# Optimization experiments

Hardware: AMD Instinct MI355X
Metric: run time of the kernel (lower is better)

The kernel has to match this reference:

```python
import jax, jax.numpy as jnp
import numpy as np

DN = ('NCHW', 'OIHW', 'NCHW')
B, H, W = 2048, 16, 16
DICT, SE, CE, ESZ, NZ = 14, 8, 16, 512, 512
EPS = 1e-4


def _conv(x, w, b):
    # 3x3 conv, padding=1 (SAME), NCHW
    return jax.lax.conv_general_dilated(x, w, (1, 1), 'SAME', dimension_numbers=DN) + b[None, :, None, None]


def _normalized(m, eps=0.0):
    return m / (jnp.sqrt(jnp.sum(m * m, axis=1, keepdims=True)) + eps)


def setup_inputs() -> dict:
    key = jax.random.key(0)
    ks = jax.random.split(key, 20)
    f = jnp.float32
    d = {
        's': jax.random.randint(ks[0], (B, H, W), 0, DICT, dtype=jnp.int32),
        's_prime': jax.random.randint(ks[1], (B, H, W), 0, DICT, dtype=jnp.int32),
        'state_embed': jax.random.normal(ks[2], (DICT, SE), f),
        'conv_embed_w': jax.random.normal(ks[3], (CE, SE, 3, 3), f) * 0.1,
        'conv_embed_b': jnp.zeros((CE,), f),
        'p1c1_w': jax.random.normal(ks[4], (16, CE, 3, 3), f) * 0.1,
        'p1c1_b': jnp.zeros((16,), f),
        'p1c2_w': jax.random.normal(ks[5], (32, 16, 3, 3), f) * 0.1,
        'p1c2_b': jnp.zeros((32,), f),
        'p1l_w': jax.random.normal(ks[6], (ESZ, 32 * H * W), f) * 0.02,
        'p1l_b': jnp.zeros((ESZ,), f),
        'p2c1_w': jax.random.normal(ks[7], (16, CE, 3, 3), f) * 0.1,
        'p2c1_b': jnp.zeros((16,), f),
        'p2c2_w': jax.random.normal(ks[8], (32, 16, 3, 3), f) * 0.1,
        'p2c2_b': jnp.zeros((32,), f),
        'p2l_w': jax.random.normal(ks[9], (ESZ, 32 * H * W), f) * 0.02,
        'p2l_b': jnp.zeros((ESZ,), f),
        'z_vectors': jax.random.normal(ks[10], (NZ, ESZ), f),
        'scale': jnp.ones((1,), f),
        'downscale_factor': 1,
    }
    return d


def _embed(s, state_embed, conv_embed_w, conv_embed_b):
    # nn.Embedding(max_norm=1): renorm rows to L2 norm <= 1 before lookup
    norms = jnp.sqrt(jnp.sum(state_embed * state_embed, axis=1, keepdims=True))
    table = state_embed / jnp.maximum(norms, 1.0)
    x = table[s]  # (B, H, W, SE)
    x = jnp.transpose(x, (0, 3, 1, 2))  # (B, SE, H, W)
    return _conv(x, conv_embed_w, conv_embed_b)


def _tower(x, c1w, c1b, c2w, c2b, lw, lb):
    x = jax.nn.relu(_conv(x, c1w, c1b))
    x = jax.nn.relu(_conv(x, c2w, c2b))
    x = x.reshape(x.shape[0], -1)  # (B, 32*H*W)
    x = x @ lw.T + lb
    return _normalized(x, EPS)


def reference(s, s_prime, state_embed, conv_embed_w, conv_embed_b,
              p1c1_w, p1c1_b, p1c2_w, p1c2_b, p1l_w, p1l_b,
              p2c1_w, p2c1_b, p2c2_w, p2c2_b, p2l_w, p2l_b,
              z_vectors, scale, downscale_factor):
    s_e = _embed(s, state_embed, conv_embed_w, conv_embed_b)
    sp_e = _embed(s_prime, state_embed, conv_embed_w, conv_embed_b)
    embed1 = _tower(s_e, p1c1_w, p1c1_b, p1c2_w, p1c2_b, p1l_w, p1l_b)
    embed2 = _tower(sp_e - s_e, p2c1_w, p2c1_b, p2c2_w, p2c2_b, p2l_w, p2l_b)
    # VQ: cosine-similarity nearest codebook vector
    zn = _normalized(z_vectors, 0.0)  # (NZ, ESZ)
    z_inds = jnp.argmax(embed2 @ zn.T, axis=1)  # (B,)
    z_matrix = zn[z_inds]  # (B, ESZ)
    if downscale_factor == 1:
        ipm = embed1 @ z_matrix.T  # (B, B)
    else:
        bs = embed1.shape[0] // downscale_factor
        v1 = embed1[::downscale_factor]  # (bs, ESZ)
        v2 = z_matrix.reshape(bs, downscale_factor, -1)
        ipm = jnp.einsum('be,bde->bd', v1, v2)
    return jnp.exp(scale) * ipm
```

## Files before the change

### kernel.cpp

```cpp
#include <hip/hip_runtime.h>
#include <math.h>


typedef __attribute__((ext_vector_type(8))) __bf16 bf16x8;
typedef __attribute__((ext_vector_type(4))) float f32x4;
typedef __attribute__((ext_vector_type(8))) unsigned short ushort8;
typedef __attribute__((ext_vector_type(4))) unsigned short ushort4v;

static __device__ __forceinline__ unsigned short f2bf(float x) {
  union { float f; unsigned u; } v; v.f = x;
  return (unsigned short)(v.u >> 16);
}
static __device__ __forceinline__ float bf2f(unsigned short h) {
  union { float f; unsigned u; } v; v.u = ((unsigned)h) << 16;
  return v.f;
}
template<int NS>
static __device__ __forceinline__ void split3(float x, unsigned short* h) {
  unsigned short q0 = f2bf(x); h[0] = q0;
  float r1 = x - bf2f(q0);
  unsigned short q1 = f2bf(r1); h[1] = q1;
  if constexpr (NS == 3) h[2] = f2bf(r1 - bf2f(q1));
}
static __device__ __forceinline__ void gload_lds16(const void* g, void* l) {
  __builtin_amdgcn_global_load_lds(
      (const __attribute__((address_space(1))) unsigned int*)g,
      (__attribute__((address_space(3))) unsigned int*)l, 16, 0, 0);
}
#define MFMA16(a, b, c) __builtin_amdgcn_mfma_f32_16x16x32_bf16((a), (b), (c), 0, 0, 0)

template<int NS>
static __device__ __forceinline__ f32x4 mfma_prod(const bf16x8* a, const bf16x8* b, f32x4 c) {
  c = MFMA16(a[0], b[0], c);
  c = MFMA16(a[0], b[1], c);
  c = MFMA16(a[1], b[0], c);
  if constexpr (NS == 3) {
    c = MFMA16(a[1], b[1], c);
    c = MFMA16(a[0], b[2], c);
    c = MFMA16(a[2], b[0], c);
  }
  return c;
}
static __device__ __forceinline__ int conv_a16(int cell, int half) {
  return (cell * 2 + half) ^ ((cell >> 2) & 7);
}
static __device__ __forceinline__ unsigned long long score_key(float v, int col) {
  unsigned b = __float_as_uint(v);
  unsigned m = b ^ ((unsigned)((int)b >> 31) | 0x80000000u);
  return ((unsigned long long)m << 32) | (unsigned)(511 - col);
}
static __device__ __forceinline__ unsigned long long shfl_xor_u64(unsigned long long v, int m) {
  unsigned lo = __shfl_xor((unsigned)v, m, 64);
  unsigned hi = __shfl_xor((unsigned)(v >> 32), m, 64);
  return ((unsigned long long)hi << 32) | lo;
}

__global__ __launch_bounds__(256) void prep_misc_kernel(
    const float* __restrict__ se, float* __restrict__ tbl,
    const float* __restrict__ zv,
    unsigned short* __restrict__ zn0, unsigned short* __restrict__ zn1,
    unsigned short* __restrict__ zn2,
    float* __restrict__ epre, unsigned long long* __restrict__ zi)
{
  __shared__ float wsum[4];
  const int b = blockIdx.x, t = threadIdx.x;
  if (b == 0) {
    if (t < 112) {
      int r = t >> 3;
      float ss = 0.f;
      #pragma unroll
      for (int i = 0; i < 8; ++i) { float v = se[r * 8 + i]; ss += v * v; }
      float n = fmaxf(sqrtf(ss), 1.0f);
      tbl[t] = se[t] / n;
    }
  } else if (b <= 512) {
    int row = b - 1;
    size_t base = (size_t)row * 512 + t * 2;
    float2 v = *reinterpret_cast<const float2*>(zv + base);
    float ss = v.x * v.x + v.y * v.y;
    #pragma unroll
    for (int m = 32; m >= 1; m >>= 1) ss += __shfl_xor(ss, m, 64);
    int lane = t & 63, wid = t >> 6;
    if (lane == 0) wsum[wid] = ss;
    __syncthreads();
    float tot = wsum[0] + wsum[1] + wsum[2] + wsum[3];
    float inv = 1.0f / sqrtf(tot);
    float a = v.x * inv, c = v.y * inv;
    unsigned short ha[3], hc[3];
    split3<3>(a, ha); split3<3>(c, hc);
    zn0[base] = ha[0]; zn0[base + 1] = hc[0];
    zn1[base] = ha[1]; zn1[base + 1] = hc[1];
    zn2[base] = ha[2]; zn2[base + 1] = hc[2];
  } else if (b <= 1024) {
    f32x4 z4 = {0.f, 0.f, 0.f, 0.f};
    size_t o = ((size_t)(b - 513) * 256 + t) * 8;
    *reinterpret_cast<f32x4*>(epre + o) = z4;
    *reinterpret_cast<f32x4*>(epre + o + 4) = z4;
  } else {
    int i = (b - 1025) * 256 + t;
    if (i < 2048) zi[i] = 0ull;
  }
}

__global__ __launch_bounds__(256) void prep_wt_all_kernel(
    const float* __restrict__ ew,
    const float* __restrict__ p1c1w, const float* __restrict__ p1c2w,
    const float* __restrict__ p2c1w, const float* __restrict__ p2c2w,
    unsigned short* __restrict__ wt)
{
  int gi = blockIdx.x * 256 + threadIdx.x;
  if (gi >= 50688) return;
  const float* src; int off, NSs, OC, mode;
  if (gi < 4608)       { src = ew;    off = 0;     NSs = 3; OC = 16; mode = 0; }
  else if (gi < 12288) { src = p1c1w; off = 4608;  NSs = 5; OC = 16; mode = 1; }
  else if (gi < 27648) { src = p1c2w; off = 12288; NSs = 5; OC = 32; mode = 1; }
  else if (gi < 35328) { src = p2c1w; off = 27648; NSs = 5; OC = 16; mode = 1; }
  else                 { src = p2c2w; off = 35328; NSs = 5; OC = 32; mode = 1; }
  int i = gi - off;
  int ic = i & 7;
  int r = i >> 3;
  int oc = r % OC; r /= OC;
  int kc = r & 3; r >>= 2;
  int s = r % NSs;
  int sp = r / NSs;
  int tap, icf, IC;
  if (mode == 0) { tap = s * 4 + kc; icf = ic; IC = 8; }
  else           { tap = s * 2 + (kc >> 1); icf = (kc & 1) * 8 + ic; IC = 16; }
  float w = 0.f;
  if (tap < 9) {
    int ky = tap / 3, kx = tap - ky * 3;
    w = src[((oc * IC + icf) * 3 + ky) * 3 + kx];
  }
  unsigned short h[3];
  split3<3>(w, h);
  wt[gi] = h[sp];
}

__global__ __launch_bounds__(256) void split_lin_kernel(
    const float* __restrict__ p1, const float* __restrict__ p2,
    unsigned short* __restrict__ w0, unsigned short* __restrict__ w1,
    unsigned short* __restrict__ u0, unsigned short* __restrict__ u1,
    unsigned short* __restrict__ u2)
{
  int blk = blockIdx.x;
  if (blk < 4096) {
    size_t i = ((size_t)blk * 256 + threadIdx.x) * 4;
    f32x4 v = *reinterpret_cast<const f32x4*>(p1 + i);
    ushort4v a, b;
    #pragma unroll
    for (int j = 0; j < 4; ++j) {
      unsigned short h[3];
      split3<2>(v[j], h);
      a[j] = h[0]; b[j] = h[1];
    }
    *reinterpret_cast<ushort4v*>(w0 + i) = a;
    *reinterpret_cast<ushort4v*>(w1 + i) = b;
  } else {
    size_t i = ((size_t)(blk - 4096) * 256 + threadIdx.x) * 4;
    f32x4 v = *reinterpret_cast<const f32x4*>(p2 + i);
    ushort4v a, b, c;
    #pragma unroll
    for (int j = 0; j < 4; ++j) {
      unsigned short h[3];
      split3<3>(v[j], h);
      a[j] = h[0]; b[j] = h[1]; c[j] = h[2];
    }
    *reinterpret_cast<ushort4v*>(u0 + i) = a;
    *reinterpret_cast<ushort4v*>(u1 + i) = b;
    *reinterpret_cast<ushort4v*>(u2 + i) = c;
  }
}

__global__ __launch_bounds__(256) void reduce_norm_kernel(
    const float* __restrict__ pre, const float* __restrict__ bias, float eps,
    unsigned short* __restrict__ o0, unsigned short* __restrict__ o1,
    unsigned short* __restrict__ o2, float* __restrict__ zero_dst)
{
  int row = blockIdx.x, t = threadIdx.x;
  size_t base = (size_t)row * 512 + t * 2;
  float2 v = *reinterpret_cast<const float2*>(pre + base);
  float ax = v.x + bias[t * 2], ay = v.y + bias[t * 2 + 1];
  float ss = ax * ax + ay * ay;
  #pragma unroll
  for (int m = 32; m >= 1; m >>= 1) ss += __shfl_xor(ss, m, 64);
  __shared__ float wsum[4];
  int lane = t & 63, wid = t >> 6;
  if (lane == 0) wsum[wid] = ss;
  __syncthreads();
  float tot = wsum[0] + wsum[1] + wsum[2] + wsum[3];
  float inv = 1.0f / (sqrtf(tot) + eps);
  float a = ax * inv, b2 = ay * inv;
  unsigned short ha[3], hb[3];
  split3<3>(a, ha); split3<3>(b2, hb);
  o0[base] = ha[0]; o0[base + 1] = hb[0];
  o1[base] = ha[1]; o1[base + 1] = hb[1];
  if (o2) { o2[base] = ha[2]; o2[base + 1] = hb[2]; }
  if (zero_dst) {
    float2 z = {0.f, 0.f};
    *reinterpret_cast<float2*>(zero_dst + base) = z;
  }
}

template<int NS>
__global__ __launch_bounds__(256) void tower_mfma_kernel(
    const int* __restrict__ sIdx, const int* __restrict__ spIdx,
    const float* __restrict__ tblf,
    const unsigned short* __restrict__ wtE,
    const unsigned short* __restrict__ wt1,
    const unsigned short* __restrict__ wt2,
    const float* __restrict__ eb, const float* __restrict__ c1b,
    const float* __restrict__ c2b,
    unsigned short* __restrict__ a0, unsigned short* __restrict__ a1,
    unsigned short* __restrict__ a2, int delta)
{
  __shared__ float tbl[112];
  __shared__ ushort8 G[NS][324];
  __shared__ ushort8 Abuf[NS][648];
  __shared__ ushort8 Bbuf[NS][648];

  const int b = blockIdx.x, t = threadIdx.x;
  const int lane = t & 63, wv = t >> 6;
  const int fr = lane & 15, kc = lane >> 4;

  if (t < 112) tbl[t] = tblf[t];
  if (t < 68) {
    int c;
    if (t < 18)      c = t;
    else if (t < 36) c = 306 + (t - 18);
    else if (t < 52) c = 18 * (t - 35);
    else             c = 18 * (t - 51) + 17;
    ushort8 z8 = {0, 0, 0, 0, 0, 0, 0, 0};
    #pragma unroll
    for (int sp = 0; sp < NS; ++sp) {
      G[sp][c] = z8;
      ((ushort8*)&Abuf[sp][0])[conv_a16(c, 0)] = z8;
      ((ushort8*)&Abuf[sp][0])[conv_a16(c, 1)] = z8;
      ((ushort8*)&Bbuf[sp][0])[conv_a16(c, 0)] = z8;
      ((ushort8*)&Bbuf[sp][0])[conv_a16(c, 1)] = z8;
    }
  }
  __syncthreads();

  {
    const int y = t >> 4, x = t & 15;
    const int cell = (y + 1) * 18 + (x + 1);
    int sv = sIdx[(size_t)b * 256 + t];
    float v[8];
    if (delta) {
      int spv = spIdx[(size_t)b * 256 + t];
      #pragma unroll
      for (int c = 0; c < 8; ++c) v[c] = tbl[spv * 8 + c] - tbl[sv * 8 + c];
    } else {
      #pragma unroll
      for (int c = 0; c < 8; ++c) v[c] = tbl[sv * 8 + c];
    }
    ushort8 h0, h1, h2;
    #pragma unroll
    for (int c = 0; c < 8; ++c) {
      unsigned short q[3];
      split3<NS>(v[c], q);
      h0[c] = q[0]; h1[c] = q[1];
      if constexpr (NS == 3) h2[c] = q[2];
    }
    G[0][cell] = h0; G[1][cell] = h1;
    if constexpr (NS == 3) G[2][cell] = h2;
  }
  __syncthreads();

  {
    float bias = 0.f;
    if (!delta) bias = eb[fr];
    f32x4 acc[4];
    #pragma unroll
    for (int j = 0; j < 4; ++j) acc[j] = (f32x4)0.f;
    #pragma unroll
    for (int s = 0; s < 3; ++s) {
      bf16x8 bw[NS];
      #pragma unroll
      for (int sp = 0; sp < NS; ++sp)
        bw[sp] = __builtin_bit_cast(bf16x8, *reinterpret_cast<const ushort8*>(
            wtE + (size_t)(((sp * 3 + s) * 4 + kc) * 16 + fr) * 8));
      int tap = s * 4 + kc; if (tap > 8) tap = 8;
      const int dy = tap / 3, dx = tap - dy * 3;
      const int cb = dy * 18 + fr + dx;
      #pragma unroll
      for (int j = 0; j < 4; ++j) {
        const int cell = cb + (wv * 4 + j) * 18;
        bf16x8 av[NS];
        #pragma unroll
        for (int sp = 0; sp < NS; ++sp)
          av[sp] = __builtin_bit_cast(bf16x8, G[sp][cell]);
        acc[j] = mfma_prod<NS>(av, bw, acc[j]);
      }
    }
    #pragma unroll
    for (int j = 0; j < 4; ++j) {
      const int y = wv * 4 + j;
      #pragma unroll
      for (int q = 0; q < 4; ++q) {
        const int x = kc * 4 + q;
        const int cell = (y + 1) * 18 + (x + 1);
        const int a16 = conv_a16(cell, fr >> 3);
        unsigned short hh[3];
        split3<NS>(acc[j][q] + bias, hh);
        #pragma unroll
        for (int sp = 0; sp < NS; ++sp)
          ((unsigned short*)&Abuf[sp][0])[a16 * 8 + (fr & 7)] = hh[sp];
      }
    }
  }
  __syncthreads();

  {
    const float bias = c1b[fr];
    f32x4 acc[4];
    #pragma unroll
    for (int j = 0; j < 4; ++j) acc[j] = (f32x4)0.f;
    #pragma unroll
    for (int s = 0; s < 5; ++s) {
      bf16x8 bw[NS];
      #pragma unroll
      for (int sp = 0; sp < NS; ++sp)
        bw[sp] = __builtin_bit_cast(bf16x8, *reinterpret_cast<const ushort8*>(
            wt1 + (size_t)(((sp * 5 + s) * 4 + kc) * 16 + fr) * 8));
      int tap = s * 2 + (kc >> 1); if (tap > 8) tap = 8;
      const int dy = tap / 3, dx = tap - dy * 3;
      const int half = kc & 1;
      const int cb = dy * 18 + fr + dx;
      #pragma unroll
      for (int j = 0; j < 4; ++j) {
        const int cell = cb + (wv * 4 + j) * 18;
        const int a16 = conv_a16(cell, half);
        bf16x8 av[NS];
        #pragma unroll
        for (int sp = 0; sp < NS; ++sp)
          av[sp] = __builtin_bit_cast(bf16x8, *reinterpret_cast<const ushort8*>(
              (const unsigned short*)&Abuf[sp][0] + a16 * 8));
        acc[j] = mfma_prod<NS>(av, bw, acc[j]);
      }
    }
    #pragma unroll
    for (int j = 0; j < 4; ++j) {
      const int y = wv * 4 + j;
      #pragma unroll
      for (int q = 0; q < 4; ++q) {
        const int x = kc * 4 + q;
        const int cell = (y + 1) * 18 + (x + 1);
        const int a16 = conv_a16(cell, fr >> 3);
        unsigned short hh[3];
        split3<NS>(fmaxf(acc[j][q] + bias, 0.f), hh);
        #pragma unroll
        for (int sp = 0; sp < NS; ++sp)
          ((unsigned short*)&Bbuf[sp][0])[a16 * 8 + (fr & 7)] = hh[sp];
      }
    }
  }
  __syncthreads();

  {
    const float bias0 = c2b[fr], bias1 = c2b[16 + fr];
    f32x4 acc0[4], acc1[4];
    #pragma unroll
    for (int j = 0; j < 4; ++j) { acc0[j] = (f32x4)0.f; acc1[j] = (f32x4)0.f; }
    #pragma unroll
    for (int s = 0; s < 5; ++s) {
      bf16x8 bw0[NS], bw1[NS];
      #pragma unroll
      for (int sp = 0; sp < NS; ++sp) {
        size_t base = (size_t)(((sp * 5 + s) * 4 + kc) * 32) * 8;
        bw0[sp] = __builtin_bit_cast(bf16x8,
            *reinterpret_cast<const ushort8*>(wt2 + base + (size_t)fr * 8));
        bw1[sp] = __builtin_bit_cast(bf16x8,
            *reinterpret_cast<const ushort8*>(wt2 + base + (size_t)(16 + fr) * 8));
      }
      int tap = s * 2 + (kc >> 1); if (tap > 8) tap = 8;
      const int dy = tap / 3, dx = tap - dy * 3;
      const int half = kc & 1;
      const int cb = dy * 18 + fr + dx;
      #pragma unroll
      for (int j = 0; j < 4; ++j) {
        const int cell = cb + (wv * 4 + j) * 18;
        const int a16 = conv_a16(cell, half);
        bf16x8 av[NS];
        #pragma unroll
        for (int sp = 0; sp < NS; ++sp)
          av[sp] = __builtin_bit_cast(bf16x8, *reinterpret_cast<const ushort8*>(
              (const unsigned short*)&Bbuf[sp][0] + a16 * 8));
        acc0[j] = mfma_prod<NS>(av, bw0, acc0[j]);
        acc1[j] = mfma_prod<NS>(av, bw1, acc1[j]);
      }
    }
    #pragma unroll
    for (int j = 0; j < 4; ++j) {
      const int y = wv * 4 + j;
      ushort4v g0[2], g1[2], g2[2];
      #pragma unroll
      for (int q = 0; q < 4; ++q) {
        unsigned short hh[3];
        split3<NS>(fmaxf(acc0[j][q] + bias0, 0.f), hh);
        g0[0][q] = hh[0]; g1[0][q] = hh[1]; if constexpr (NS == 3) g2[0][q] = hh[2];
        split3<NS>(fmaxf(acc1[j][q] + bias1, 0.f), hh);
        g0[1][q] = hh[0]; g1[1][q] = hh[1]; if constexpr (NS == 3) g2[1][q] = hh[2];
      }
      size_t base0 = (size_t)b * 8192 + (size_t)fr * 256 + y * 16 + kc * 4;
      size_t base1 = base0 + 16 * 256;
      *reinterpret_cast<ushort4v*>(a0 + base0) = g0[0];
      *reinterpret_cast<ushort4v*>(a0 + base1) = g0[1];
      *reinterpret_cast<ushort4v*>(a1 + base0) = g1[0];
      *reinterpret_cast<ushort4v*>(a1 + base1) = g1[1];
      if constexpr (NS == 3) {
        *reinterpret_cast<ushort4v*>(a2 + base0) = g2[0];
        *reinterpret_cast<ushort4v*>(a2 + base1) = g2[1];
      }
    }
  }
}

template<int NS, int EPI>
__global__ __launch_bounds__(256) void mfma_gemm_kernel(
    const unsigned short* __restrict__ A0, const unsigned short* __restrict__ A1,
    const unsigned short* __restrict__ A2,
    const unsigned short* __restrict__ B0, const unsigned short* __restrict__ B1,
    const unsigned short* __restrict__ B2,
    const unsigned long long* __restrict__ gkey,
    unsigned long long* __restrict__ zout,
    const float* __restrict__ scale_p,
    float* __restrict__ C, int M, int N, int K, int Ksub)
{
  __shared__ unsigned short ldsA[NS][4096];
  __shared__ unsigned short ldsB[NS][4096];

  const int t = threadIdx.x;
  const int lane = t & 63, wv = t >> 6;
  const int m0 = blockIdx.x * 128, n0 = blockIdx.y * 128;
  const long kbase = (long)blockIdx.z * Ksub;
  const int NT = Ksub >> 5;

  const int st_row = lane >> 2;
  const int st_cb = (lane & 3) * 16;
  int srow[2];
  long bgrow[2];
  #pragma unroll
  for (int r = 0; r < 2; ++r) {
    srow[r] = (wv + 4 * r) * 16 + st_row;
    long g = n0 + srow[r];
    if constexpr (EPI == 2)
      g = 511 - (long)(unsigned)(gkey[n0 + srow[r]] & 0xFFFFFFFFull);
    bgrow[r] = g;
  }

  const int wr = wv >> 1, wc = wv & 1;
  const int fr = lane & 15, kc = lane >> 4;

  f32x4 acc[4][4];
  #pragma unroll
  for (int mi = 0; mi < 4; ++mi)
    #pragma unroll
    for (int ni = 0; ni < 4; ++ni) acc[mi][ni] = (f32x4)0.f;

  const unsigned short* Asp[3] = {A0, A1, A2};
  const unsigned short* Bsp[3] = {B0, B1, B2};

  for (int kt = 0; kt < NT; ++kt) {
    const long k0 = kbase + (long)kt * 32;
    #pragma unroll
    for (int sp = 0; sp < NS; ++sp)
      #pragma unroll
      for (int r = 0; r < 2; ++r) {
        int row = srow[r];
        int c = st_cb ^ (((row >> 1) & 3) << 4);
        gload_lds16(Asp[sp] + (size_t)(m0 + row) * K + k0 + (c >> 1),
                    &ldsA[sp][(wv + 4 * r) * 512]);
      }
    #pragma unroll
    for (int sp = 0; sp < NS; ++sp)
      #pragma unroll
      for (int r = 0; r < 2; ++r) {
        int row = srow[r];
        int c = st_cb ^ (((row >> 1) & 3) << 4);
        gload_lds16(Bsp[sp] + (size_t)bgrow[r] * K + k0 + (c >> 1),
                    &ldsB[sp][(wv + 4 * r) * 512]);
      }
    __syncthreads();

    bf16x8 af[NS][4], bf[NS][4];
    #pragma unroll
    for (int sp = 0; sp < NS; ++sp) {
      #pragma unroll
      for (int mi = 0; mi < 4; ++mi) {
        int row = wr * 64 + mi * 16 + fr;
        int cb = (kc * 16) ^ (((row >> 1) & 3) << 4);
        af[sp][mi] = __builtin_bit_cast(bf16x8,
            *reinterpret_cast<const ushort8*>(&ldsA[sp][row * 32 + (cb >> 1)]));
      }
      #pragma unroll
      for (int ni = 0; ni < 4; ++ni) {
        int row = wc * 64 + ni * 16 + fr;
        int cb = (kc * 16) ^ (((row >> 1) & 3) << 4);
        bf[sp][ni] = __builtin_bit_cast(bf16x8,
            *reinterpret_cast<const ushort8*>(&ldsB[sp][row * 32 + (cb >> 1)]));
      }
    }
    #pragma unroll
    for (int mi = 0; mi < 4; ++mi)
      #pragma unroll
      for (int ni = 0; ni < 4; ++ni) {
        f32x4 c = acc[mi][ni];
        c = MFMA16(af[0][mi], bf[0][ni], c);
        c = MFMA16(af[0][mi], bf[1][ni], c);
        c = MFMA16(af[1][mi], bf[0][ni], c);
        if constexpr (NS == 3) {
          c = MFMA16(af[1][mi], bf[1][ni], c);
          c = MFMA16(af[0][mi], bf[2][ni], c);
          c = MFMA16(af[2][mi], bf[0][ni], c);
        }
        acc[mi][ni] = c;
      }
    __syncthreads();
  }

  if constexpr (EPI == 0) {
    #pragma unroll
    for (int mi = 0; mi < 4; ++mi)
      #pragma unroll
      for (int ni = 0; ni < 4; ++ni) {
        int col = n0 + wc * 64 + ni * 16 + fr;
        #pragma unroll
        for (int q = 0; q < 4; ++q) {
          int row = m0 + wr * 64 + mi * 16 + kc * 4 + q;
          atomicAdd(&C[(size_t)row * N + col], acc[mi][ni][q]);
        }
      }
  } else if constexpr (EPI == 2) {
    float scl = expf(scale_p[0]);
    #pragma unroll
    for (int mi = 0; mi < 4; ++mi)
      #pragma unroll
      for (int ni = 0; ni < 4; ++ni) {
        int col = n0 + wc * 64 + ni * 16 + fr;
        #pragma unroll
        for (int q = 0; q < 4; ++q) {
          int row = m0 + wr * 64 + mi * 16 + kc * 4 + q;
          C[(size_t)row * N + col] = acc[mi][ni][q] * scl;
        }
      }
  } else {
    #pragma unroll
    for (int mi = 0; mi < 4; ++mi)
      #pragma unroll
      for (int q = 0; q < 4; ++q) {
        int row = m0 + wr * 64 + mi * 16 + kc * 4 + q;
        unsigned long long best = 0ull;
        #pragma unroll
        for (int ni = 0; ni < 4; ++ni) {
          int col = n0 + wc * 64 + ni * 16 + fr;
          unsigned long long k2 = score_key(acc[mi][ni][q], col);
          best = (k2 > best) ? k2 : best;
        }
        #pragma unroll
        for (int m2 = 1; m2 < 16; m2 <<= 1) {
          unsigned long long o = shfl_xor_u64(best, m2);
          best = (o > best) ? o : best;
        }
        if (fr == 0) atomicMax(zout + row, best);
      }
  }
}

extern "C" void kernel_launch(void* const* d_in, const int* in_sizes, int n_in,
                              void* d_out, int out_size, void* d_ws, size_t ws_size,
                              hipStream_t stream)
{
  const int*   s      = (const int*)  d_in[0];
  const int*   sprime = (const int*)  d_in[1];
  const float* se     = (const float*)d_in[2];
  const float* ew     = (const float*)d_in[3];
  const float* eb     = (const float*)d_in[4];
  const float* p1c1w  = (const float*)d_in[5];
  const float* p1c1b  = (const float*)d_in[6];
  const float* p1c2w  = (const float*)d_in[7];
  const float* p1c2b  = (const float*)d_in[8];
  const float* p1lw   = (const float*)d_in[9];
  const float* p1lb   = (const float*)d_in[10];
  const float* p2c1w  = (const float*)d_in[11];
  const float* p2c1b  = (const float*)d_in[12];
  const float* p2c2w  = (const float*)d_in[13];
  const float* p2c2b  = (const float*)d_in[14];
  const float* p2lw   = (const float*)d_in[15];
  const float* p2lb   = (const float*)d_in[16];
  const float* zv     = (const float*)d_in[17];
  const float* scale  = (const float*)d_in[18];
  float* out = (float*)d_out;

  char* w = (char*)d_ws;
  size_t off = 0;
  auto alloc = [&](size_t bytes) -> char* {
    char* p = w + off;
    off += (bytes + 255) & ~(size_t)255;
    return p;
  };
  float* tblf = (float*)alloc(112 * 4);
  unsigned short* zn0 = (unsigned short*)alloc((size_t)512 * 512 * 2);
  unsigned short* zn1 = (unsigned short*)alloc((size_t)512 * 512 * 2);
  unsigned short* zn2 = (unsigned short*)alloc((size_t)512 * 512 * 2);
  unsigned short* e10 = (unsigned short*)alloc((size_t)2048 * 512 * 2);
  unsigned short* e11 = (unsigned short*)alloc((size_t)2048 * 512 * 2);
  unsigned short* e20 = (unsigned short*)alloc((size_t)2048 * 512 * 2);
  unsigned short* e21 = (unsigned short*)alloc((size_t)2048 * 512 * 2);
  unsigned short* e22 = (unsigned short*)alloc((size_t)2048 * 512 * 2);
  float* epre = (float*)alloc((size_t)2048 * 512 * 4);
  unsigned long long* zi = (unsigned long long*)alloc(2048 * 8);
  unsigned short* wt = (unsigned short*)alloc((size_t)50688 * 2);
  unsigned short* act0 = (unsigned short*)alloc((size_t)2048 * 8192 * 2);
  unsigned short* act1 = (unsigned short*)alloc((size_t)2048 * 8192 * 2);
  unsigned short* act2 = (unsigned short*)alloc((size_t)2048 * 8192 * 2);
  unsigned short* u0 = (unsigned short*)alloc((size_t)512 * 8192 * 2);
  unsigned short* u1 = (unsigned short*)alloc((size_t)512 * 8192 * 2);
  unsigned short* u2 = (unsigned short*)alloc((size_t)512 * 8192 * 2);
  unsigned short* w0 = act2;
  unsigned short* w1 = act2 + (size_t)512 * 8192;

  unsigned short* wtE  = wt;
  unsigned short* wt1a = wt + 4608;
  unsigned short* wt2a = wt + 12288;
  unsigned short* wt1b = wt + 27648;
  unsigned short* wt2b = wt + 35328;

  prep_misc_kernel<<<1033, 256, 0, stream>>>(se, tblf, zv, zn0, zn1, zn2, epre, zi);
  prep_wt_all_kernel<<<198, 256, 0, stream>>>(ew, p1c1w, p1c2w, p2c1w, p2c2w, wt);
  split_lin_kernel<<<8192, 256, 0, stream>>>(p1lw, p2lw, w0, w1, u0, u1, u2);

  tower_mfma_kernel<2><<<2048, 256, 0, stream>>>(
      s, sprime, tblf, wtE, wt1a, wt2a, eb, p1c1b, p1c2b, act0, act1, act2, 0);
  mfma_gemm_kernel<2, 0><<<dim3(16, 4, 8), 256, 0, stream>>>(
      act0, act1, nullptr, w0, w1, nullptr, nullptr, nullptr,
      nullptr, epre, 2048, 512, 8192, 1024);
  reduce_norm_kernel<<<2048, 256, 0, stream>>>(epre, p1lb, 1e-4f,
                                               e10, e11, nullptr, epre);

  tower_mfma_kernel<3><<<2048, 256, 0, stream>>>(
      s, sprime, tblf, wtE, wt1b, wt2b, eb, p2c1b, p2c2b, act0, act1, act2, 1);
  mfma_gemm_kernel<3, 0><<<dim3(16, 4, 8), 256, 0, stream>>>(
      act0, act1, act2, u0, u1, u2, nullptr, nullptr,
      nullptr, epre, 2048, 512, 8192, 1024);
  reduce_norm_kernel<<<2048, 256, 0, stream>>>(epre, p2lb, 1e-4f,
                                               e20, e21, e22, nullptr);

  mfma_gemm_kernel<3, 3><<<dim3(16, 4, 1), 256, 0, stream>>>(
      e20, e21, e22, zn0, zn1, zn2, nullptr, zi, nullptr,
      nullptr, 2048, 512, 512, 512);
  mfma_gemm_kernel<2, 2><<<dim3(16, 16, 1), 256, 0, stream>>>(
      e10, e11, nullptr, zn0, zn1, nullptr, zi, nullptr, scale,
      out, 2048, 2048, 512, 512);
}
```

Measured before the change: 474.1 us.

## Load GEMM B fragments directly from global and merge prep kernels

```diff
diff --git a/kernel.cpp b/kernel.cpp
--- a/kernel.cpp
+++ b/kernel.cpp
@@ -26,6 +26,9 @@
   __builtin_amdgcn_global_load_lds(
       (const __attribute__((address_space(1))) unsigned int*)g,
       (__attribute__((address_space(3))) unsigned int*)l, 16, 0, 0);
+}
+static __device__ __forceinline__ bf16x8 gfrag(const unsigned short* p) {
+  return __builtin_bit_cast(bf16x8, *reinterpret_cast<const ushort8*>(p));
 }
 #define MFMA16(a, b, c) __builtin_amdgcn_mfma_f32_16x16x32_bf16((a), (b), (c), 0, 0, 0)
 
@@ -55,12 +58,20 @@
   return ((unsigned long long)hi << 32) | lo;
 }
 
-__global__ __launch_bounds__(256) void prep_misc_kernel(
+__global__ __launch_bounds__(256) void prep_all_kernel(
     const float* __restrict__ se, float* __restrict__ tbl,
     const float* __restrict__ zv,
     unsigned short* __restrict__ zn0, unsigned short* __restrict__ zn1,
     unsigned short* __restrict__ zn2,
-    float* __restrict__ epre, unsigned long long* __restrict__ zi)
+    float* __restrict__ epre, unsigned long long* __restrict__ zi,
+    const float* __restrict__ ew,
+    const float* __restrict__ p1c1w, const float* __restrict__ p1c2w,
+    const float* __restrict__ p2c1w, const float* __restrict__ p2c2w,
+    unsigned short* __restrict__ wt,
+    const float* __restrict__ p1lw, const float* __restrict__ p2lw,
+    unsigned short* __restrict__ w0, unsigned short* __restrict__ w1,
+    unsigned short* __restrict__ u0, unsigned short* __restrict__ u1,
+    unsigned short* __restrict__ u2)
 {
   __shared__ float wsum[4];
   const int b = blockIdx.x, t = threadIdx.x;
@@ -96,78 +107,64 @@
     size_t o = ((size_t)(b - 513) * 256 + t) * 8;
     *reinterpret_cast<f32x4*>(epre + o) = z4;
     *reinterpret_cast<f32x4*>(epre + o + 4) = z4;
-  } else {
+  } else if (b <= 1032) {
     int i = (b - 1025) * 256 + t;
     if (i < 2048) zi[i] = 0ull;
-  }
-}
-
-__global__ __launch_bounds__(256) void prep_wt_all_kernel(
-    const float* __restrict__ ew,
-    const float* __restrict__ p1c1w, const float* __restrict__ p1c2w,
-    const float* __restrict__ p2c1w, const float* __restrict__ p2c2w,
-    unsigned short* __restrict__ wt)
-{
-  int gi = blockIdx.x * 256 + threadIdx.x;
-  if (gi >= 50688) return;
-  const float* src; int off, NSs, OC, mode;
-  if (gi < 4608)       { src = ew;    off = 0;     NSs = 3; OC = 16; mode = 0; }
-  else if (gi < 12288) { src = p1c1w; off = 4608;  NSs = 5; OC = 16; mode = 1; }
-  else if (gi < 27648) { src = p1c2w; off = 12288; NSs = 5; OC = 32; mode = 1; }
-  else if (gi < 35328) { src = p2c1w; off = 27648; NSs = 5; OC = 16; mode = 1; }
-  else                 { src = p2c2w; off = 35328; NSs = 5; OC = 32; mode = 1; }
-  int i = gi - off;
-  int ic = i & 7;
-  int r = i >> 3;
-  int oc = r % OC; r /= OC;
-  int kc = r & 3; r >>= 2;
-  int s = r % NSs;
-  int sp = r / NSs;
-  int tap, icf, IC;
-  if (mode == 0) { tap = s * 4 + kc; icf = ic; IC = 8; }
-  else           { tap = s * 2 + (kc >> 1); icf = (kc & 1) * 8 + ic; IC = 16; }
-  float w = 0.f;
-  if (tap < 9) {
-    int ky = tap / 3, kx = tap - ky * 3;
-    w = src[((oc * IC + icf) * 3 + ky) * 3 + kx];
-  }
-  unsigned short h[3];
-  split3<3>(w, h);
-  wt[gi] = h[sp];
-}
-
-__global__ __launch_bounds__(256) void split_lin_kernel(
-    const float* __restrict__ p1, const float* __restrict__ p2,
-    unsigned short* __restrict__ w0, unsigned short* __restrict__ w1,
-    unsigned short* __restrict__ u0, unsigned short* __restrict__ u1,
-    unsigned short* __restrict__ u2)
-{
-  int blk = blockIdx.x;
-  if (blk < 4096) {
-    size_t i = ((size_t)blk * 256 + threadIdx.x) * 4;
-    f32x4 v = *reinterpret_cast<const f32x4*>(p1 + i);
-    ushort4v a, b;
-    #pragma unroll
-    for (int j = 0; j < 4; ++j) {
-      unsigned short h[3];
-      split3<2>(v[j], h);
-      a[j] = h[0]; b[j] = h[1];
-    }
-    *reinterpret_cast<ushort4v*>(w0 + i) = a;
-    *reinterpret_cast<ushort4v*>(w1 + i) = b;
+  } else if (b <= 1230) {
+    int gi = (b - 1033) * 256 + t;
+    if (gi >= 50688) return;
+    const float* src; int off, NSs, OC, mode;
+    if (gi < 4608)       { src = ew;    off = 0;     NSs = 3; OC = 16; mode = 0; }
+    else if (gi < 12288) { src = p1c1w; off = 4608;  NSs = 5; OC = 16; mode = 1; }
+    else if (gi < 27648) { src = p1c2w; off = 12288; NSs = 5; OC = 32; mode = 1; }
+    else if (gi < 35328) { src = p2c1w; off = 27648; NSs = 5; OC = 16; mode = 1; }
+    else                 { src = p2c2w; off = 35328; NSs = 5; OC = 32; mode = 1; }
+    int i = gi - off;
+    int ic = i & 7;
+    int r = i >> 3;
+    int oc = r % OC; r /= OC;
+    int kc = r & 3; r >>= 2;
+    int s = r % NSs;
+    int sp = r / NSs;
+    int tap, icf, IC;
+    if (mode == 0) { tap = s * 4 + kc; icf = ic; IC = 8; }
+    else           { tap = s * 2 + (kc >> 1); icf = (kc & 1) * 8 + ic; IC = 16; }
+    float w = 0.f;
+    if (tap < 9) {
+      int ky = tap / 3, kx = tap - ky * 3;
+      w = src[((oc * IC + icf) * 3 + ky) * 3 + kx];
+    }
+    unsigned short h[3];
+    split3<3>(w, h);
+    wt[gi] = h[sp];
   } else {
-    size_t i = ((size_t)(blk - 4096) * 256 + threadIdx.x) * 4;
-    f32x4 v = *reinterpret_cast<const f32x4*>(p2 + i);
-    ushort4v a, b, c;
-    #pragma unroll
-    for (int j = 0; j < 4; ++j) {
-      unsigned short h[3];
-      split3<3>(v[j], h);
-      a[j] = h[0]; b[j] = h[1]; c[j] = h[2];
-    }
-    *reinterpret_cast<ushort4v*>(u0 + i) = a;
-    *reinterpret_cast<ushort4v*>(u1 + i) = b;
-    *reinterpret_cast<ushort4v*>(u2 + i) = c;
+    int blk = b - 1231;
+    if (blk < 4096) {
+      size_t i = ((size_t)blk * 256 + t) * 4;
+      f32x4 v = *reinterpret_cast<const f32x4*>(p1lw + i);
+      ushort4v a, b2;
+      #pragma unroll
+      for (int j = 0; j < 4; ++j) {
+        unsigned short h[3];
+        split3<2>(v[j], h);
+        a[j] = h[0]; b2[j] = h[1];
+      }
+      *reinterpret_cast<ushort4v*>(w0 + i) = a;
+      *reinterpret_cast<ushort4v*>(w1 + i) = b2;
+    } else {
+      size_t i = ((size_t)(blk - 4096) * 256 + t) * 4;
+      f32x4 v = *reinterpret_cast<const f32x4*>(p2lw + i);
+      ushort4v a, b2, c;
+      #pragma unroll
+      for (int j = 0; j < 4; ++j) {
+        unsigned short h[3];
+        split3<3>(v[j], h);
+        a[j] = h[0]; b2[j] = h[1]; c[j] = h[2];
+      }
+      *reinterpret_cast<ushort4v*>(u0 + i) = a;
+      *reinterpret_cast<ushort4v*>(u1 + i) = b2;
+      *reinterpret_cast<ushort4v*>(u2 + i) = c;
+    }
   }
 }
 
@@ -417,7 +414,7 @@
 }
 
 template<int NS, int EPI>
-__global__ __launch_bounds__(256) void mfma_gemm_kernel(
+__global__ __launch_bounds__(256, 4) void mfma_gemm_kernel(
     const unsigned short* __restrict__ A0, const unsigned short* __restrict__ A1,
     const unsigned short* __restrict__ A2,
     const unsigned short* __restrict__ B0, const unsigned short* __restrict__ B1,
@@ -428,7 +425,6 @@
     float* __restrict__ C, int M, int N, int K, int Ksub)
 {
   __shared__ unsigned short ldsA[NS][4096];
-  __shared__ unsigned short ldsB[NS][4096];
 
   const int t = threadIdx.x;
   const int lane = t & 63, wv = t >> 6;
@@ -439,18 +435,20 @@
   const int st_row = lane >> 2;
   const int st_cb = (lane & 3) * 16;
   int srow[2];
-  long bgrow[2];
   #pragma unroll
-  for (int r = 0; r < 2; ++r) {
-    srow[r] = (wv + 4 * r) * 16 + st_row;
-    long g = n0 + srow[r];
-    if constexpr (EPI == 2)
-      g = 511 - (long)(unsigned)(gkey[n0 + srow[r]] & 0xFFFFFFFFull);
-    bgrow[r] = g;
-  }
+  for (int r = 0; r < 2; ++r) srow[r] = (wv + 4 * r) * 16 + st_row;
 
   const int wr = wv >> 1, wc = wv & 1;
   const int fr = lane & 15, kc = lane >> 4;
+
+  size_t brow[4];
+  #pragma unroll
+  for (int ni = 0; ni < 4; ++ni) {
+    int col = n0 + wc * 64 + ni * 16 + fr;
+    long g = col;
+    if constexpr (EPI == 2) g = 511 - (long)(unsigned)(gkey[col] & 0xFFFFFFFFull);
+    brow[ni] = (size_t)g * K;
+  }
 
   f32x4 acc[4][4];
   #pragma unroll
@@ -459,7 +457,6 @@
     for (int ni = 0; ni < 4; ++ni) acc[mi][ni] = (f32x4)0.f;
 
   const unsigned short* Asp[3] = {A0, A1, A2};
-  const unsigned short* Bsp[3] = {B0, B1, B2};
 
   for (int kt = 0; kt < NT; ++kt) {
     const long k0 = kbase + (long)kt * 32;
@@ -472,20 +469,11 @@
         gload_lds16(Asp[sp] + (size_t)(m0 + row) * K + k0 + (c >> 1),
                     &ldsA[sp][(wv + 4 * r) * 512]);
       }
+    __syncthreads();
+
+    bf16x8 af[NS][4];
     #pragma unroll
     for (int sp = 0; sp < NS; ++sp)
-      #pragma unroll
-      for (int r = 0; r < 2; ++r) {
-        int row = srow[r];
-        int c = st_cb ^ (((row >> 1) & 3) << 4);
-        gload_lds16(Bsp[sp] + (size_t)bgrow[r] * K + k0 + (c >> 1),
-                    &ldsB[sp][(wv + 4 * r) * 512]);
-      }
-    __syncthreads();
-
-    bf16x8 af[NS][4], bf[NS][4];
-    #pragma unroll
-    for (int sp = 0; sp < NS; ++sp) {
       #pragma unroll
       for (int mi = 0; mi < 4; ++mi) {
         int row = wr * 64 + mi * 16 + fr;
@@ -493,29 +481,49 @@
         af[sp][mi] = __builtin_bit_cast(bf16x8,
             *reinterpret_cast<const ushort8*>(&ldsA[sp][row * 32 + (cb >> 1)]));
       }
-      #pragma unroll
-      for (int ni = 0; ni < 4; ++ni) {
-        int row = wc * 64 + ni * 16 + fr;
-        int cb = (kc * 16) ^ (((row >> 1) & 3) << 4);
-        bf[sp][ni] = __builtin_bit_cast(bf16x8,
-            *reinterpret_cast<const ushort8*>(&ldsB[sp][row * 32 + (cb >> 1)]));
-      }
-    }
+
+    const long koff = k0 + kc * 8;
+    bf16x8 bb[4];
+    #pragma unroll
+    for (int ni = 0; ni < 4; ++ni) bb[ni] = gfrag(B0 + brow[ni] + koff);
     #pragma unroll
     for (int mi = 0; mi < 4; ++mi)
       #pragma unroll
-      for (int ni = 0; ni < 4; ++ni) {
-        f32x4 c = acc[mi][ni];
-        c = MFMA16(af[0][mi], bf[0][ni], c);
-        c = MFMA16(af[0][mi], bf[1][ni], c);
-        c = MFMA16(af[1][mi], bf[0][ni], c);
-        if constexpr (NS == 3) {
-          c = MFMA16(af[1][mi], bf[1][ni], c);
-          c = MFMA16(af[0][mi], bf[2][ni], c);
-          c = MFMA16(af[2][mi], bf[0][ni], c);
-        }
-        acc[mi][ni] = c;
-      }
+      for (int ni = 0; ni < 4; ++ni)
+        acc[mi][ni] = MFMA16(af[0][mi], bb[ni], acc[mi][ni]);
+    #pragma unroll
+    for (int mi = 0; mi < 4; ++mi)
+      #pragma unroll
+      for (int ni = 0; ni < 4; ++ni)
+        acc[mi][ni] = MFMA16(af[1][mi], bb[ni], acc[mi][ni]);
+    if constexpr (NS == 3) {
+      #pragma unroll
+      for (int mi = 0; mi < 4; ++mi)
+        #pragma unroll
+        for (int ni = 0; ni < 4; ++ni)
+          acc[mi][ni] = MFMA16(af[2][mi], bb[ni], acc[mi][ni]);
+    }
+    #pragma unroll
+    for (int ni = 0; ni < 4; ++ni) bb[ni] = gfrag(B1 + brow[ni] + koff);
+    #pragma unroll
+    for (int mi = 0; mi < 4; ++mi)
+      #pragma unroll
+      for (int ni = 0; ni < 4; ++ni)
+        acc[mi][ni] = MFMA16(af[0][mi], bb[ni], acc[mi][ni]);
+    if constexpr (NS == 3) {
+      #pragma unroll
+      for (int mi = 0; mi < 4; ++mi)
+        #pragma unroll
+        for (int ni = 0; ni < 4; ++ni)
+          acc[mi][ni] = MFMA16(af[1][mi], bb[ni], acc[mi][ni]);
+      #pragma unroll
+      for (int ni = 0; ni < 4; ++ni) bb[ni] = gfrag(B2 + brow[ni] + koff);
+      #pragma unroll
+      for (int mi = 0; mi < 4; ++mi)
+        #pragma unroll
+        for (int ni = 0; ni < 4; ++ni)
+          acc[mi][ni] = MFMA16(af[0][mi], bb[ni], acc[mi][ni]);
+    }
     __syncthreads();
   }
 
@@ -626,9 +634,10 @@
   unsigned short* wt1b = wt + 27648;
   unsigned short* wt2b = wt + 35328;
 
-  prep_misc_kernel<<<1033, 256, 0, stream>>>(se, tblf, zv, zn0, zn1, zn2, epre, zi);
-  prep_wt_all_kernel<<<198, 256, 0, stream>>>(ew, p1c1w, p1c2w, p2c1w, p2c2w, wt);
-  split_lin_kernel<<<8192, 256, 0, stream>>>(p1lw, p2lw, w0, w1, u0, u1, u2);
+  prep_all_kernel<<<9423, 256, 0, stream>>>(
+      se, tblf, zv, zn0, zn1, zn2, epre, zi,
+      ew, p1c1w, p1c2w, p2c1w, p2c2w, wt,
+      p1lw, p2lw, w0, w1, u0, u1, u2);
 
   tower_mfma_kernel<2><<<2048, 256, 0, stream>>>(
       s, sprime, tblf, wtE, wt1a, wt2a, eb, p1c1b, p1c2b, act0, act1, act2, 0);
```

New measurement: 688.0 us. 1.45x slower.

## Merge prep kernels into one launch and prefetch next GEMM K-tile during MFMA

Applied to the files above, without the earlier changes.

```diff
diff --git a/kernel.cpp b/kernel.cpp
--- a/kernel.cpp
+++ b/kernel.cpp
@@ -55,12 +55,20 @@
   return ((unsigned long long)hi << 32) | lo;
 }
 
-__global__ __launch_bounds__(256) void prep_misc_kernel(
+__global__ __launch_bounds__(256) void prep_all_kernel(
     const float* __restrict__ se, float* __restrict__ tbl,
     const float* __restrict__ zv,
     unsigned short* __restrict__ zn0, unsigned short* __restrict__ zn1,
     unsigned short* __restrict__ zn2,
-    float* __restrict__ epre, unsigned long long* __restrict__ zi)
+    float* __restrict__ epre, unsigned long long* __restrict__ zi,
+    const float* __restrict__ ew,
+    const float* __restrict__ p1c1w, const float* __restrict__ p1c2w,
+    const float* __restrict__ p2c1w, const float* __restrict__ p2c2w,
+    unsigned short* __restrict__ wt,
+    const float* __restrict__ p1lw, const float* __restrict__ p2lw,
+    unsigned short* __restrict__ w0, unsigned short* __restrict__ w1,
+    unsigned short* __restrict__ u0, unsigned short* __restrict__ u1,
+    unsigned short* __restrict__ u2)
 {
   __shared__ float wsum[4];
   const int b = blockIdx.x, t = threadIdx.x;
@@ -96,78 +104,64 @@
     size_t o = ((size_t)(b - 513) * 256 + t) * 8;
     *reinterpret_cast<f32x4*>(epre + o) = z4;
     *reinterpret_cast<f32x4*>(epre + o + 4) = z4;
-  } else {
+  } else if (b <= 1032) {
     int i = (b - 1025) * 256 + t;
     if (i < 2048) zi[i] = 0ull;
-  }
-}
-
-__global__ __launch_bounds__(256) void prep_wt_all_kernel(
-    const float* __restrict__ ew,
-    const float* __restrict__ p1c1w, const float* __restrict__ p1c2w,
-    const float* __restrict__ p2c1w, const float* __restrict__ p2c2w,
-    unsigned short* __restrict__ wt)
-{
-  int gi = blockIdx.x * 256 + threadIdx.x;
-  if (gi >= 50688) return;
-  const float* src; int off, NSs, OC, mode;
-  if (gi < 4608)       { src = ew;    off = 0;     NSs = 3; OC = 16; mode = 0; }
-  else if (gi < 12288) { src = p1c1w; off = 4608;  NSs = 5; OC = 16; mode = 1; }
-  else if (gi < 27648) { src = p1c2w; off = 12288; NSs = 5; OC = 32; mode = 1; }
-  else if (gi < 35328) { src = p2c1w; off = 27648; NSs = 5; OC = 16; mode = 1; }
-  else                 { src = p2c2w; off = 35328; NSs = 5; OC = 32; mode = 1; }
-  int i = gi - off;
-  int ic = i & 7;
-  int r = i >> 3;
-  int oc = r % OC; r /= OC;
-  int kc = r & 3; r >>= 2;
-  int s = r % NSs;
-  int sp = r / NSs;
-  int tap, icf, IC;
-  if (mode == 0) { tap = s * 4 + kc; icf = ic; IC = 8; }
-  else           { tap = s * 2 + (kc >> 1); icf = (kc & 1) * 8 + ic; IC = 16; }
-  float w = 0.f;
-  if (tap < 9) {
-    int ky = tap / 3, kx = tap - ky * 3;
-    w = src[((oc * IC + icf) * 3 + ky) * 3 + kx];
-  }
-  unsigned short h[3];
-  split3<3>(w, h);
-  wt[gi] = h[sp];
-}
-
-__global__ __launch_bounds__(256) void split_lin_kernel(
-    const float* __restrict__ p1, const float* __restrict__ p2,
-    unsigned short* __restrict__ w0, unsigned short* __restrict__ w1,
-    unsigned short* __restrict__ u0, unsigned short* __restrict__ u1,
-    unsigned short* __restrict__ u2)
-{
-  int blk = blockIdx.x;
-  if (blk < 4096) {
-    size_t i = ((size_t)blk * 256 + threadIdx.x) * 4;
-    f32x4 v = *reinterpret_cast<const f32x4*>(p1 + i);
-    ushort4v a, b;
-    #pragma unroll
-    for (int j = 0; j < 4; ++j) {
-      unsigned short h[3];
-      split3<2>(v[j], h);
-      a[j] = h[0]; b[j] = h[1];
-    }
-    *reinterpret_cast<ushort4v*>(w0 + i) = a;
-    *reinterpret_cast<ushort4v*>(w1 + i) = b;
+  } else if (b <= 1230) {
+    int gi = (b - 1033) * 256 + t;
+    if (gi >= 50688) return;
+    const float* src; int off, NSs, OC, mode;
+    if (gi < 4608)       { src = ew;    off = 0;     NSs = 3; OC = 16; mode = 0; }
+    else if (gi < 12288) { src = p1c1w; off = 4608;  NSs = 5; OC = 16; mode = 1; }
+    else if (gi < 27648) { src = p1c2w; off = 12288; NSs = 5; OC = 32; mode = 1; }
+    else if (gi < 35328) { src = p2c1w; off = 27648; NSs = 5; OC = 16; mode = 1; }
+    else                 { src = p2c2w; off = 35328; NSs = 5; OC = 32; mode = 1; }
+    int i = gi - off;
+    int ic = i & 7;
+    int r = i >> 3;
+    int oc = r % OC; r /= OC;
+    int kc = r & 3; r >>= 2;
+    int s = r % NSs;
+    int sp = r / NSs;
+    int tap, icf, IC;
+    if (mode == 0) { tap = s * 4 + kc; icf = ic; IC = 8; }
+    else           { tap = s * 2 + (kc >> 1); icf = (kc & 1) * 8 + ic; IC = 16; }
+    float w = 0.f;
+    if (tap < 9) {
+      int ky = tap / 3, kx = tap - ky * 3;
+      w = src[((oc * IC + icf) * 3 + ky) * 3 + kx];
+    }
+    unsigned short h[3];
+    split3<3>(w, h);
+    wt[gi] = h[sp];
   } else {
-    size_t i = ((size_t)(blk - 4096) * 256 + threadIdx.x) * 4;
-    f32x4 v = *reinterpret_cast<const f32x4*>(p2 + i);
-    ushort4v a, b, c;
-    #pragma unroll
-    for (int j = 0; j < 4; ++j) {
-      unsigned short h[3];
-      split3<3>(v[j], h);
-      a[j] = h[0]; b[j] = h[1]; c[j] = h[2];
-    }
-    *reinterpret_cast<ushort4v*>(u0 + i) = a;
-    *reinterpret_cast<ushort4v*>(u1 + i) = b;
-    *reinterpret_cast<ushort4v*>(u2 + i) = c;
+    int blk = b - 1231;
+    if (blk < 4096) {
+      size_t i = ((size_t)blk * 256 + t) * 4;
+      f32x4 v = *reinterpret_cast<const f32x4*>(p1lw + i);
+      ushort4v a, b2;
+      #pragma unroll
+      for (int j = 0; j < 4; ++j) {
+        unsigned short h[3];
+        split3<2>(v[j], h);
+        a[j] = h[0]; b2[j] = h[1];
+      }
+      *reinterpret_cast<ushort4v*>(w0 + i) = a;
+      *reinterpret_cast<ushort4v*>(w1 + i) = b2;
+    } else {
+      size_t i = ((size_t)(blk - 4096) * 256 + t) * 4;
+      f32x4 v = *reinterpret_cast<const f32x4*>(p2lw + i);
+      ushort4v a, b2, c;
+      #pragma unroll
+      for (int j = 0; j < 4; ++j) {
+        unsigned short h[3];
+        split3<3>(v[j], h);
+        a[j] = h[0]; b2[j] = h[1]; c[j] = h[2];
+      }
+      *reinterpret_cast<ushort4v*>(u0 + i) = a;
+      *reinterpret_cast<ushort4v*>(u1 + i) = b2;
+      *reinterpret_cast<ushort4v*>(u2 + i) = c;
+    }
   }
 }
 
@@ -461,7 +455,7 @@
   const unsigned short* Asp[3] = {A0, A1, A2};
   const unsigned short* Bsp[3] = {B0, B1, B2};
 
-  for (int kt = 0; kt < NT; ++kt) {
+  auto stage = [&](int kt) {
     const long k0 = kbase + (long)kt * 32;
     #pragma unroll
     for (int sp = 0; sp < NS; ++sp)
@@ -471,16 +465,13 @@
         int c = st_cb ^ (((row >> 1) & 3) << 4);
         gload_lds16(Asp[sp] + (size_t)(m0 + row) * K + k0 + (c >> 1),
                     &ldsA[sp][(wv + 4 * r) * 512]);
-      }
-    #pragma unroll
-    for (int sp = 0; sp < NS; ++sp)
-      #pragma unroll
-      for (int r = 0; r < 2; ++r) {
-        int row = srow[r];
-        int c = st_cb ^ (((row >> 1) & 3) << 4);
         gload_lds16(Bsp[sp] + (size_t)bgrow[r] * K + k0 + (c >> 1),
                     &ldsB[sp][(wv + 4 * r) * 512]);
       }
+  };
+
+  stage(0);
+  for (int kt = 0; kt < NT; ++kt) {
     __syncthreads();
 
     bf16x8 af[NS][4], bf[NS][4];
@@ -501,6 +492,10 @@
             *reinterpret_cast<const ushort8*>(&ldsB[sp][row * 32 + (cb >> 1)]));
       }
     }
+    __syncthreads();
+
+    if (kt + 1 < NT) stage(kt + 1);
+
     #pragma unroll
     for (int mi = 0; mi < 4; ++mi)
       #pragma unroll
@@ -516,7 +511,6 @@
         }
         acc[mi][ni] = c;
       }
-    __syncthreads();
   }
 
   if constexpr (EPI == 0) {
@@ -626,9 +620,10 @@
   unsigned short* wt1b = wt + 27648;
   unsigned short* wt2b = wt + 35328;
 
-  prep_misc_kernel<<<1033, 256, 0, stream>>>(se, tblf, zv, zn0, zn1, zn2, epre, zi);
-  prep_wt_all_kernel<<<198, 256, 0, stream>>>(ew, p1c1w, p1c2w, p2c1w, p2c2w, wt);
-  split_lin_kernel<<<8192, 256, 0, stream>>>(p1lw, p2lw, w0, w1, u0, u1, u2);
+  prep_all_kernel<<<9423, 256, 0, stream>>>(
+      se, tblf, zv, zn0, zn1, zn2, epre, zi,
+      ew, p1c1w, p1c2w, p2c1w, p2c2w, wt,
+      p1lw, p2lw, w0, w1, u0, u1, u2);
 
   tower_mfma_kernel<2><<<2048, 256, 0, stream>>>(
       s, sprime, tblf, wtE, wt1a, wt2a, eb, p1c1b, p1c2b, act0, act1, act2, 0);
```

New measurement: 446.8 us. 1.06x faster.
